# Performance work log

Measured on AMD Instinct MI355X. Metric: run time of the kernel, lower is better.

Reference implementation:

```python
import jax, jax.numpy as jnp
import numpy as np
from jax import lax

B, NPG, IN, OUT, ETYPES, STEPS, E = 16, 1024, 128, 256, 2, 6, 262144
N = B * NPG
CONCAT = IN + OUT
EPS = 1e-5


def setup_inputs() -> dict:
    key = jax.random.key(0)
    ks = jax.random.split(key, 24)
    s = 0.05
    return {
        "features": jax.random.normal(ks[0], (N, IN), jnp.float32),
        "src": jax.random.randint(ks[1], (E,), 0, N, jnp.int32),
        "dst": jax.random.randint(ks[2], (E,), 0, N, jnp.int32),
        "etype": jax.random.randint(ks[3], (E,), 0, ETYPES, jnp.int32),
        # GGNN per-etype linears (weight, bias) and GRUCell params
        "W_lin": jax.random.normal(ks[4], (ETYPES, OUT, OUT), jnp.float32) * s,
        "b_lin": jnp.zeros((ETYPES, OUT), jnp.float32),
        "W_ih": jax.random.normal(ks[5], (3 * OUT, OUT), jnp.float32) * s,
        "W_hh": jax.random.normal(ks[6], (3 * OUT, OUT), jnp.float32) * s,
        "b_ih": jnp.zeros((3 * OUT,), jnp.float32),
        "b_hh": jnp.zeros((3 * OUT,), jnp.float32),
        # conv branch on h_i (OUT channels)
        "conv1_w": jax.random.normal(ks[7], (OUT, OUT, 3), jnp.float32) * s,
        "conv1_b": jnp.zeros((OUT,), jnp.float32),
        "conv2_w": jax.random.normal(ks[8], (OUT, OUT, 1), jnp.float32) * s,
        "conv2_b": jnp.zeros((OUT,), jnp.float32),
        # conv branch on c_i (CONCAT channels)
        "convc1_w": jax.random.normal(ks[9], (CONCAT, CONCAT, 3), jnp.float32) * s,
        "convc1_b": jnp.zeros((CONCAT,), jnp.float32),
        "convc2_w": jax.random.normal(ks[10], (CONCAT, CONCAT, 1), jnp.float32) * s,
        "convc2_b": jnp.zeros((CONCAT,), jnp.float32),
        # shared batchnorms (training-mode batch stats, affine params)
        "bn_g": jnp.ones((OUT,), jnp.float32),
        "bn_b": jnp.zeros((OUT,), jnp.float32),
        "bnc_g": jnp.ones((CONCAT,), jnp.float32),
        "bnc_b": jnp.zeros((CONCAT,), jnp.float32),
        # gating MLPs
        "mlpy_w": jax.random.normal(ks[11], (2, OUT), jnp.float32) * s,
        "mlpy_b": jnp.zeros((2,), jnp.float32),
        "mlpz_w": jax.random.normal(ks[12], (2, CONCAT), jnp.float32) * s,
        "mlpz_b": jnp.zeros((2,), jnp.float32),
    }


def _bn_relu(x, g, b):  # x: [B, C, L], training-mode BN (biased var)
    mean = x.mean(axis=(0, 2), keepdims=True)
    var = ((x - mean) ** 2).mean(axis=(0, 2), keepdims=True)
    xn = (x - mean) * lax.rsqrt(var + EPS)
    return jax.nn.relu(xn * g[None, :, None] + b[None, :, None])


def _conv1d(x, w, b):  # x: [B, C, L], w: [O, I, K]
    y = lax.conv_general_dilated(x, w, (1,), 'VALID',
                                 dimension_numbers=('NCH', 'OIH', 'NCH'))
    return y + b[None, :, None]


def _maxpool(x, k, s):
    return lax.reduce_window(x, -jnp.inf, lax.max, (1, 1, k), (1, 1, s), 'VALID')


def _forward(features, src, dst, etype, W_lin, b_lin, W_ih, W_hh, b_ih, b_hh,
             conv1_w, conv1_b, conv2_w, conv2_b, convc1_w, convc1_b,
             convc2_w, convc2_b, bn_g, bn_b, bnc_g, bnc_b,
             mlpy_w, mlpy_b, mlpz_w, mlpz_b):
    # --- GatedGraphConv (DGL semantics): pad, n_steps of msg-pass + GRUCell ---
    h = jnp.pad(features, ((0, 0), (0, OUT - IN)))  # [N, OUT]
    for _ in range(STEPS):
        # per-etype linear applied to all nodes: [ETYPES, N, OUT]
        Wh = jnp.einsum('nd,ekd->enk', h, W_lin) + b_lin[:, None, :]
        msg = Wh[etype, src]                              # [E, OUT] gather
        agg = jax.ops.segment_sum(msg, dst, num_segments=N)  # scatter-add
        gi = agg @ W_ih.T + b_ih
        gh = h @ W_hh.T + b_hh
        ir, iz, ig = jnp.split(gi, 3, axis=-1)
        hr, hz, hg = jnp.split(gh, 3, axis=-1)
        r = jax.nn.sigmoid(ir + hr)
        z = jax.nn.sigmoid(iz + hz)
        n = jnp.tanh(ig + r * hg)
        h = (1.0 - z) * n + z * h

    h_i = h.reshape(B, NPG, OUT)
    x_i = features.reshape(B, NPG, IN)
    c_i = jnp.concatenate([h_i, x_i], axis=-1)  # [B, NPG, CONCAT]

    hT = jnp.swapaxes(h_i, 1, 2)  # [B, OUT, NPG]
    Y1 = _maxpool(_bn_relu(_conv1d(hT, conv1_w, conv1_b), bn_g, bn_b), 3, 2)
    Y2 = jnp.swapaxes(_maxpool(_bn_relu(_conv1d(Y1, conv2_w, conv2_b), bn_g, bn_b), 2, 2), 1, 2)

    cT = jnp.swapaxes(c_i, 1, 2)  # [B, CONCAT, NPG]
    Z1 = _maxpool(_bn_relu(_conv1d(cT, convc1_w, convc1_b), bnc_g, bnc_b), 3, 2)
    Z2 = jnp.swapaxes(_maxpool(_bn_relu(_conv1d(Z1, convc2_w, convc2_b), bnc_g, bnc_b), 2, 2), 1, 2)

    before_avg = (Y2 @ mlpy_w.T + mlpy_b) * (Z2 @ mlpz_w.T + mlpz_b)  # [B, L, 2]
    return jax.nn.sigmoid(before_avg.mean(axis=1))  # [B, 2]


def reference(features, src, dst, etype, W_lin, b_lin, W_ih, W_hh, b_ih, b_hh,
              conv1_w, conv1_b, conv2_w, conv2_b, convc1_w, convc1_b,
              convc2_w, convc2_b, bn_g, bn_b, bnc_g, bnc_b,
              mlpy_w, mlpy_b, mlpz_w, mlpz_b):
    return _forward(features, src, dst, etype, W_lin, b_lin, W_ih, W_hh, b_ih, b_hh,
                    conv1_w, conv1_b, conv2_w, conv2_b, convc1_w, convc1_b,
                    convc2_w, convc2_b, bn_g, bn_b, bnc_g, bnc_b,
                    mlpy_w, mlpy_b, mlpz_w, mlpz_b)
```

## Files before the change

### kernel.cpp

```cpp
#include <hip/hip_runtime.h>
#include <math.h>

constexpr int Bn     = 16;
constexpr int NPG    = 1024;
constexpr int Nn     = Bn * NPG;
constexpr int FIN    = 128;
constexpr int FOUT   = 256;
constexpr int CCAT   = 384;
constexpr int STEPS  = 6;
constexpr int NE     = 262144;

using short8 = __attribute__((ext_vector_type(8))) short;
using f32x4  = __attribute__((ext_vector_type(4))) float;

static __device__ __forceinline__ unsigned short f2bf(float x) {
    union { float f; unsigned u; } v; v.f = x;
    unsigned r = (v.u + 0x7FFFu + ((v.u >> 16) & 1u)) >> 16;
    return (unsigned short)r;
}
static __device__ __forceinline__ float bf2f(unsigned short b) {
    union { unsigned u; float f; } v; v.u = ((unsigned)b) << 16;
    return v.f;
}
static __device__ __forceinline__ float sigm(float x) { return 1.f / (1.f + expf(-x)); }

static __device__ __forceinline__ void gload16(const void* g, void* l) {
    __builtin_amdgcn_global_load_lds(
        (const __attribute__((address_space(1))) void*)g,
        (__attribute__((address_space(3))) void*)l, 16, 0, 0);
}


__global__ void cvt_bf(const float* __restrict__ s, unsigned short* __restrict__ d, int n) {
    int i = blockIdx.x * 256 + threadIdx.x;
    if (i < n) d[i] = f2bf(s[i]);
}

__global__ void cvt_wcat(const float* __restrict__ Wih, const float* __restrict__ Whh,
                         unsigned short* __restrict__ Wcat) {
    int o = blockIdx.x * 256 + threadIdx.x;
    int k = o >> 9, j = o & 511;
    float v = (j < 256) ? Whh[(size_t)k * 256 + j] : Wih[(size_t)k * 256 + (j - 256)];
    Wcat[o] = f2bf(v);
}

__global__ void add_bias(const float* __restrict__ a, const float* __restrict__ b,
                         float* __restrict__ o, int n) {
    int i = blockIdx.x * 256 + threadIdx.x;
    if (i < n) o[i] = a[i] + b[i];
}

__global__ void cvt_wconv(const float* __restrict__ W, unsigned short* __restrict__ Wt,
                          int C, int KW, int n) {
    int o = blockIdx.x * 256 + threadIdx.x;
    if (o >= n) return;
    int c = o / (KW * C), rem = o % (KW * C);
    int kb = rem / C, i = rem % C;
    Wt[o] = f2bf(W[(size_t)(c * C + i) * KW + kb]);
}

__global__ void pad_h(const float* __restrict__ f, float* __restrict__ h,
                      unsigned short* __restrict__ Acat) {
    int i = blockIdx.x * 256 + threadIdx.x;
    int k = i & 255, n = i >> 8;
    float v = (k < FIN) ? f[(size_t)n * FIN + k] : 0.f;
    h[i] = v; Acat[(size_t)n * 512 + k] = f2bf(v);
}

__global__ void build_cb(const unsigned short* __restrict__ Acat, const float* __restrict__ f,
                         unsigned short* __restrict__ cb) {
    int idx = blockIdx.x * 256 + threadIdx.x;
    int c = idx % CCAT, n = idx / CCAT;
    cb[idx] = (c < FOUT) ? Acat[(size_t)n * 512 + c] : f2bf(f[(size_t)n * FIN + (c - FOUT)]);
}


__global__ void edge_count(const int* __restrict__ dst, int* __restrict__ deg) {
    int e = blockIdx.x * 256 + threadIdx.x;
    atomicAdd(&deg[dst[e]], 1);
}

__global__ __launch_bounds__(1024) void scan_deg(const int* __restrict__ deg,
                                                 int* __restrict__ rowptr,
                                                 int* __restrict__ cursor) {
    __shared__ int ps[1024];
    const int t = threadIdx.x;
    int loc[16]; int s = 0;
    const int base = t * 16;
#pragma unroll
    for (int i = 0; i < 16; ++i) { loc[i] = deg[base + i]; s += loc[i]; }
    ps[t] = s;
    __syncthreads();
    for (int off = 1; off < 1024; off <<= 1) {
        int add = (t >= off) ? ps[t - off] : 0;
        __syncthreads();
        ps[t] += add;
        __syncthreads();
    }
    int run = ps[t] - s;
#pragma unroll
    for (int i = 0; i < 16; ++i) { rowptr[base + i] = run; cursor[base + i] = run; run += loc[i]; }
    if (t == 1023) rowptr[16384] = run;
}

__global__ void edge_fill(const int* __restrict__ src, const int* __restrict__ dst,
                          const int* __restrict__ et, int* __restrict__ cursor,
                          int* __restrict__ widx) {
    int e = blockIdx.x * 256 + threadIdx.x;
    int slot = atomicAdd(&cursor[dst[e]], 1);
    widx[slot] = src[e] * 2 + et[e];
}

static __device__ __forceinline__ void gemm128_body(
    const unsigned short* __restrict__ Ab, const unsigned short* __restrict__ W,
    const float* __restrict__ bias, float* __restrict__ Cf,
    unsigned short* __restrict__ Cb, int Ctap, int lda, int L, int Lv, int N, int K,
    int outBf, int l0, int col0, unsigned short* As, unsigned short* Bs) {
    const int t = threadIdx.x;
    const int w = t >> 6, l = t & 63;
    const int lr = l & 15, lhi = l >> 4;
    const int wr = w >> 1, wc = w & 1;
    const int srow8 = l >> 3;
    const int scole = ((l & 7) ^ srow8) * 8;
    const int lx7 = l & 7;

    f32x4 acc[4][4] = {};

    for (int k0 = 0; k0 < K; k0 += 64) {
        const int kb = k0 / Ctap;
        const int i0 = k0 - kb * Ctap;
        __syncthreads();
#pragma unroll
        for (int p = 0; p < 4; ++p) {
            const int r = w * 32 + p * 8;
            int srow = l0 + r + srow8 + kb;
            srow = srow < L ? srow : L - 1;
            gload16(Ab + (size_t)srow * lda + i0 + scole, &As[r * 64]);
            gload16(W + (size_t)(col0 + r + srow8) * K + k0 + scole, &Bs[r * 64]);
        }
        __syncthreads();
        const int abase = (wr * 64 + lr) * 64;
        const int bbase = (wc * 64 + lr) * 64;
#pragma unroll
        for (int kk = 0; kk < 2; ++kk) {
            const int soff = ((kk * 4 + lhi) ^ lx7) * 8;
            short8 af[4], bw[4];
#pragma unroll
            for (int fi = 0; fi < 4; ++fi)
                af[fi] = *(const short8*)&As[abase + fi * 1024 + soff];
#pragma unroll
            for (int fj = 0; fj < 4; ++fj)
                bw[fj] = *(const short8*)&Bs[bbase + fj * 1024 + soff];
#pragma unroll
            for (int fi = 0; fi < 4; ++fi)
#pragma unroll
                for (int fj = 0; fj < 4; ++fj)
                    acc[fi][fj] = __builtin_amdgcn_mfma_f32_16x16x32_bf16(
                        af[fi], bw[fj], acc[fi][fj], 0, 0, 0);
        }
    }
    const int rb = lhi * 4;
#pragma unroll
    for (int fi = 0; fi < 4; ++fi)
#pragma unroll
        for (int fj = 0; fj < 4; ++fj) {
            const int gcol = col0 + wc * 64 + fj * 16 + lr;
            const float bv = bias[gcol];
#pragma unroll
            for (int rr = 0; rr < 4; ++rr) {
                const int grow = l0 + wr * 64 + fi * 16 + rb + rr;
                if (grow < Lv) {
                    float v = acc[fi][fj][rr] + bv;
                    const size_t o = (size_t)grow * N + gcol;
                    if (outBf) Cb[o] = f2bf(v);
                    else       Cf[o] = v;
                }
            }
        }
}

__global__ __launch_bounds__(256) void gemm128(
    const unsigned short* __restrict__ A, const unsigned short* __restrict__ W,
    const float* __restrict__ bias, float* __restrict__ Cf,
    unsigned short* __restrict__ Cb, int Ctap, int lda, int L, int Lv, int N, int K,
    int outBf) {
    __shared__ unsigned short As[128 * 64];
    __shared__ unsigned short Bs[128 * 64];
    const size_t zo = (size_t)blockIdx.z;
    gemm128_body(A + zo * (size_t)L * lda, W, bias,
                 Cf ? Cf + zo * (size_t)Lv * N : nullptr,
                 Cb ? Cb + zo * (size_t)Lv * N : nullptr,
                 Ctap, lda, L, Lv, N, K, outBf,
                 blockIdx.y * 128, blockIdx.x * 128, As, Bs);
}

__global__ __launch_bounds__(256) void gemm128_swz(
    const unsigned short* __restrict__ A, const unsigned short* __restrict__ W,
    const float* __restrict__ bias, unsigned short* __restrict__ Cb,
    int lda, int N, int K) {
    __shared__ unsigned short As[128 * 64];
    __shared__ unsigned short Bs[128 * 64];
    const int gX = gridDim.x;
    const int hId = blockIdx.x + gX * blockIdx.y;
    const int xcd = hId & 7, tt = hId >> 3;
    const int bx = tt % gX, by = xcd + 8 * (tt / gX);
    gemm128_body(A, W, bias, nullptr, Cb, lda, lda, Nn, Nn, N, K, 1,
                 by * 128, bx * 128, As, Bs);
}

__global__ __launch_bounds__(256) void gemm_gru(
    const unsigned short* __restrict__ Acat, const unsigned short* __restrict__ Wcat,
    const unsigned short* __restrict__ Whg, const float* __restrict__ bias_s,
    const float* __restrict__ bias_g, float* __restrict__ h,
    unsigned short* __restrict__ Anext) {
    __shared__ unsigned short As[64 * 64];
    __shared__ unsigned short Bs[256 * 64];
    const int hId = blockIdx.x + 4 * blockIdx.y;
    const int xcd = hId & 7, tt = hId >> 3;
    const int bx = tt & 3, by = xcd + 8 * (tt >> 2);
    const int l0 = by * 64, c0 = bx * 64;

    const int t = threadIdx.x;
    const int w = t >> 6, l = t & 63;
    const int lr = l & 15, lhi = l >> 4;
    const int srow8 = l >> 3;
    const int scole = ((l & 7) ^ srow8) * 8;
    const int lx7 = l & 7;

    f32x4 acc[16] = {};

#pragma unroll
    for (int k0 = 0; k0 < 512; k0 += 64) {
        __syncthreads();
#pragma unroll
        for (int p = 0; p < 2; ++p) {
            const int r = w * 16 + p * 8;
            gload16(Acat + (size_t)(l0 + r + srow8) * 512 + k0 + scole, &As[r * 64]);
        }
#pragma unroll
        for (int p = 0; p < 8; ++p) {
            const int r = w * 64 + p * 8;
            if (r < 192) {
                const int g = r >> 6;
                const int cr = (r & 63) + srow8;
                gload16(Wcat + (size_t)(g * 256 + c0 + cr) * 512 + k0 + scole, &Bs[r * 64]);
            } else if (k0 < 256) {
                const int cr = (r - 192) + srow8;
                gload16(Whg + (size_t)(c0 + cr) * 256 + k0 + scole, &Bs[r * 64]);
            }
        }
        __syncthreads();
        const int abase = (w * 16 + lr) * 64;
#pragma unroll
        for (int kk = 0; kk < 2; ++kk) {
            const int soff = ((kk * 4 + lhi) ^ lx7) * 8;
            short8 a0 = *(const short8*)&As[abase + soff];
#pragma unroll
            for (int g = 0; g < 4; ++g) {
                if (!(g == 3 && k0 >= 256)) {
#pragma unroll
                    for (int fj = 0; fj < 4; ++fj) {
                        short8 bb = *(const short8*)&Bs[(g * 64 + fj * 16 + lr) * 64 + soff];
                        acc[g * 4 + fj] = __builtin_amdgcn_mfma_f32_16x16x32_bf16(
                            a0, bb, acc[g * 4 + fj], 0, 0, 0);
                    }
                }
            }
        }
    }
    const int rb = lhi * 4;
#pragma unroll
    for (int fj = 0; fj < 4; ++fj) {
        const int c = c0 + fj * 16 + lr;
        const float br = bias_s[c];
        const float bz = bias_s[256 + c];
        const float bg = bias_s[512 + c];
        const float bh = bias_g[c];
#pragma unroll
        for (int rr = 0; rr < 4; ++rr) {
            const int grow = l0 + w * 16 + rb + rr;
            float sr = acc[0 * 4 + fj][rr] + br;
            float sz = acc[1 * 4 + fj][rr] + bz;
            float sg = acc[2 * 4 + fj][rr] + bg;
            float hg = acc[3 * 4 + fj][rr] + bh;
            float r = sigm(sr), z = sigm(sz);
            float nn = tanhf(sg - (1.f - r) * hg);
            const size_t ho = (size_t)grow * 256 + c;
            float hv = (1.f - z) * nn + z * h[ho];
            h[ho] = hv;
            Anext[(size_t)grow * 512 + c] = f2bf(hv);
        }
    }
}

__global__ __launch_bounds__(64) void gather_agg(
    const unsigned short* __restrict__ Whb, const int* __restrict__ rowptr,
    const int* __restrict__ widx, unsigned short* __restrict__ Acat) {
    const int n = blockIdx.x, t = threadIdx.x;
    float a0 = 0, a1 = 0, a2 = 0, a3 = 0;
    const int s0 = rowptr[n], s1 = rowptr[n + 1];
    for (int s = s0; s < s1; ++s) {
        const ushort4 v = *(const ushort4*)(Whb + (size_t)widx[s] * 256 + t * 4);
        a0 += bf2f(v.x); a1 += bf2f(v.y); a2 += bf2f(v.z); a3 += bf2f(v.w);
    }
    ushort4 o; o.x = f2bf(a0); o.y = f2bf(a1); o.z = f2bf(a2); o.w = f2bf(a3);
    *(ushort4*)(Acat + (size_t)n * 512 + 256 + t * 4) = o;
}

constexpr int NCHUNK = 128;
__global__ __launch_bounds__(256) void bn_part_cl(
    const float* __restrict__ X, float* __restrict__ pS, float* __restrict__ pQ,
    int C, int totalRows, int rowsPerChunk) {
    const int t  = threadIdx.x;
    const int cq = t & 31, rl = t >> 5;
    const int c0 = blockIdx.x * 128 + cq * 4;
    const int r0 = blockIdx.y * rowsPerChunk;
    const int r1 = min(r0 + rowsPerChunk, totalRows);
    float s0 = 0, s1 = 0, s2 = 0, s3 = 0, q0 = 0, q1 = 0, q2 = 0, q3 = 0;
    for (int r = r0 + rl; r < r1; r += 8) {
        float4 v = *(const float4*)(X + (size_t)r * C + c0);
        s0 += v.x; s1 += v.y; s2 += v.z; s3 += v.w;
        q0 += v.x * v.x; q1 += v.y * v.y; q2 += v.z * v.z; q3 += v.w * v.w;
    }
    __shared__ float ls[8][128], lq[8][128];
    ls[rl][cq * 4 + 0] = s0; ls[rl][cq * 4 + 1] = s1;
    ls[rl][cq * 4 + 2] = s2; ls[rl][cq * 4 + 3] = s3;
    lq[rl][cq * 4 + 0] = q0; lq[rl][cq * 4 + 1] = q1;
    lq[rl][cq * 4 + 2] = q2; lq[rl][cq * 4 + 3] = q3;
    __syncthreads();
    if (rl == 0) {
#pragma unroll
        for (int i = 0; i < 4; ++i) {
            const int c = cq * 4 + i;
            float ss = 0, qq = 0;
#pragma unroll
            for (int j = 0; j < 8; ++j) { ss += ls[j][c]; qq += lq[j][c]; }
            pS[(size_t)blockIdx.y * C + c0 + i] = ss;
            pQ[(size_t)blockIdx.y * C + c0 + i] = qq;
        }
    }
}

__global__ __launch_bounds__(128) void bn_reduce_cl(
    const float* __restrict__ pS, const float* __restrict__ pQ,
    float* __restrict__ mean, float* __restrict__ var, int C, int totalRows) {
    const int c = blockIdx.x, t = threadIdx.x;
    __shared__ float rs[128], rq[128];
    rs[t] = pS[(size_t)t * C + c];
    rq[t] = pQ[(size_t)t * C + c];
    __syncthreads();
    for (int st = 64; st; st >>= 1) {
        if (t < st) { rs[t] += rs[t + st]; rq[t] += rq[t + st]; }
        __syncthreads();
    }
    if (t == 0) {
        float m = rs[0] / totalRows;
        mean[c] = m;
        var[c]  = rq[0] / totalRows - m * m;
    }
}

__global__ void bnp_cl(const float* __restrict__ X, const float* __restrict__ mean,
                       const float* __restrict__ var, const float* __restrict__ g,
                       const float* __restrict__ bta, float* __restrict__ Of,
                       unsigned short* __restrict__ Ob, int C, int Lin, int Lout,
                       int Kp, int outBf) {
    int idx = blockIdx.x * 256 + threadIdx.x;
    if (idx >= Bn * Lout * C) return;
    int c = idx % C, j = (idx / C) % Lout, b = idx / (C * Lout);
    float sc = g[c] * rsqrtf(var[c] + 1e-5f);
    float sh = bta[c] - mean[c] * sc;
    const float* xb = X + ((size_t)b * Lin + j * 2) * C + c;
    float m = 0.f;
    for (int k = 0; k < Kp; ++k) m = fmaxf(m, xb[(size_t)k * C] * sc + sh);
    if (outBf) Ob[idx] = f2bf(m);
    else       Of[idx] = m;
}

__global__ void final_dot(const float* __restrict__ Y2, const float* __restrict__ Z2,
                          const float* __restrict__ wy, const float* __restrict__ by,
                          const float* __restrict__ wz, const float* __restrict__ bz,
                          float* __restrict__ prod) {
    const int b = blockIdx.y, j = blockIdx.x, t = threadIdx.x;
    float p0 = 0, p1 = 0, q0 = 0, q1 = 0;
    const float* yrow = Y2 + (size_t)(b * 255 + j) * FOUT;
    const float* zrow = Z2 + (size_t)(b * 255 + j) * CCAT;
    for (int c = t; c < FOUT; c += 128) {
        float v = yrow[c];
        p0 += v * wy[c]; p1 += v * wy[FOUT + c];
    }
    for (int c = t; c < CCAT; c += 128) {
        float v = zrow[c];
        q0 += v * wz[c]; q1 += v * wz[CCAT + c];
    }
    __shared__ float r0[128], r1[128], r2[128], r3[128];
    r0[t] = p0; r1[t] = p1; r2[t] = q0; r3[t] = q1;
    __syncthreads();
    for (int s = 64; s; s >>= 1) {
        if (t < s) { r0[t] += r0[t + s]; r1[t] += r1[t + s]; r2[t] += r2[t + s]; r3[t] += r3[t + s]; }
        __syncthreads();
    }
    if (t == 0) {
        float y0 = r0[0] + by[0], y1 = r1[0] + by[1];
        float z0 = r2[0] + bz[0], z1 = r3[0] + bz[1];
        prod[((size_t)b * 255 + j) * 2 + 0] = y0 * z0;
        prod[((size_t)b * 255 + j) * 2 + 1] = y1 * z1;
    }
}

__global__ void final_out(const float* __restrict__ prod, float* __restrict__ out) {
    const int b = blockIdx.x, t = threadIdx.x;
    const int w = t >> 6, lane = t & 63;
    float s = 0.f;
    for (int j = lane; j < 255; j += 64) s += prod[((size_t)b * 255 + j) * 2 + w];
#pragma unroll
    for (int off = 32; off; off >>= 1) s += __shfl_down(s, off);
    if (lane == 0) out[b * 2 + w] = 1.f / (1.f + expf(-s / 255.f));
}

extern "C" void kernel_launch(void* const* d_in, const int* in_sizes, int n_in,
                              void* d_out, int out_size, void* d_ws, size_t ws_size,
                              hipStream_t stream) {
    (void)in_sizes; (void)n_in; (void)out_size; (void)ws_size;
    const float* features = (const float*)d_in[0];
    const int*   src      = (const int*)d_in[1];
    const int*   dst      = (const int*)d_in[2];
    const int*   etype    = (const int*)d_in[3];
    const float* W_lin    = (const float*)d_in[4];
    const float* b_lin    = (const float*)d_in[5];
    const float* W_ih     = (const float*)d_in[6];
    const float* W_hh     = (const float*)d_in[7];
    const float* b_ih     = (const float*)d_in[8];
    const float* b_hh     = (const float*)d_in[9];
    const float* conv1_w  = (const float*)d_in[10];
    const float* conv1_b  = (const float*)d_in[11];
    const float* conv2_w  = (const float*)d_in[12];
    const float* conv2_b  = (const float*)d_in[13];
    const float* convc1_w = (const float*)d_in[14];
    const float* convc1_b = (const float*)d_in[15];
    const float* convc2_w = (const float*)d_in[16];
    const float* convc2_b = (const float*)d_in[17];
    const float* bn_g     = (const float*)d_in[18];
    const float* bn_b     = (const float*)d_in[19];
    const float* bnc_g    = (const float*)d_in[20];
    const float* bnc_b    = (const float*)d_in[21];
    const float* mlpy_w   = (const float*)d_in[22];
    const float* mlpy_b   = (const float*)d_in[23];
    const float* mlpz_w   = (const float*)d_in[24];
    const float* mlpz_b   = (const float*)d_in[25];

    float* ws = (float*)d_ws;
    float*          h      = ws;
    unsigned short* Acat0  = (unsigned short*)(ws + 4194304);
    float*          bufA   = ws + 8388608;
    float*          bufB   = ws + 20971520;
    unsigned short* Wlin_b = (unsigned short*)(ws + 33554432);
    unsigned short* Whh_b  = (unsigned short*)(ws + 33554432) + 131072;
    unsigned short* Wcat_b = (unsigned short*)(ws + 33554432) + 327680;
    float*          bias_s = ws + 33950000;
    int*            ib     = (int*)(ws + 34000000);
    int* deg    = ib;
    int* cursor = ib + 16384;
    int* rowptr = ib + 32768;
    int* widx   = ib + 49160;
    float* sreg = ws + 34500000;
    float* meanb = sreg;
    float* varb  = sreg + 384;
    float* pS    = sreg + 1024;
    float* pQ    = sreg + 50176;
    float* prod  = sreg + 99328;

    unsigned short* Whb   = (unsigned short*)bufA;
    unsigned short* Acat1 = (unsigned short*)(bufA + 4194304);
    const unsigned short* Whg = Whh_b + 512 * 256;

    cvt_bf<<<512,  256, 0, stream>>>(W_lin, Wlin_b, 131072);
    cvt_bf<<<768,  256, 0, stream>>>(W_hh,  Whh_b,  196608);
    cvt_wcat<<<1536, 256, 0, stream>>>(W_ih, W_hh, Wcat_b);
    add_bias<<<3, 256, 0, stream>>>(b_ih, b_hh, bias_s, 768);
    pad_h<<<Nn * FOUT / 256, 256, 0, stream>>>(features, h, Acat0);

    hipMemsetAsync(deg, 0, 16384 * sizeof(int), stream);
    edge_count<<<NE / 256, 256, 0, stream>>>(dst, deg);
    scan_deg<<<1, 1024, 0, stream>>>(deg, rowptr, cursor);
    edge_fill<<<NE / 256, 256, 0, stream>>>(src, dst, etype, cursor, widx);

    unsigned short* Acur = Acat0;
    unsigned short* Anxt = Acat1;
    for (int s6 = 0; s6 < STEPS; ++s6) {
        gemm128_swz<<<dim3(4, 128), 256, 0, stream>>>(
            Acur, Wlin_b, b_lin, Whb, 512, 512, 256);
        gather_agg<<<Nn, 64, 0, stream>>>(Whb, rowptr, widx, Acur);
        gemm_gru<<<dim3(4, 256), 256, 0, stream>>>(
            Acur, Wcat_b, Whg, bias_s, b_hh + 512, h, Anxt);
        unsigned short* tmp = Acur; Acur = Anxt; Anxt = tmp;
    }

    unsigned short* cb    = (unsigned short*)ws;
    float*          Yc1   = bufA;
    unsigned short* P1y   = (unsigned short*)(bufA + 4186112);
    float*          Yc2   = bufA + 5230592;
    float*          Y2    = bufA + 7319552;
    float*          Z2    = bufA + 8364032;
    float*          Zc1   = bufB;
    unsigned short* P1z   = (unsigned short*)(bufB + 6279168);
    float*          Zc2   = bufB + 7845888;
    unsigned short* Wcv   = (unsigned short*)(bufB + 11000000);
    unsigned short* c1b   = Wcv;
    unsigned short* c2b   = Wcv + 196608;
    unsigned short* cc1b  = Wcv + 262144;
    unsigned short* cc2b  = Wcv + 704512;

    cvt_wconv<<<768,  256, 0, stream>>>(conv1_w,  c1b,  FOUT, 3, FOUT * FOUT * 3);
    cvt_wconv<<<256,  256, 0, stream>>>(conv2_w,  c2b,  FOUT, 1, FOUT * FOUT);
    cvt_wconv<<<1728, 256, 0, stream>>>(convc1_w, cc1b, CCAT, 3, CCAT * CCAT * 3);
    cvt_wconv<<<576,  256, 0, stream>>>(convc2_w, cc2b, CCAT, 1, CCAT * CCAT);
    build_cb<<<Nn * CCAT / 256, 256, 0, stream>>>(Acat0, features, cb);

    const int rows1 = Bn * 1022;
    const int rows2 = Bn * 510;
    const int rpc1  = (rows1 + NCHUNK - 1) / NCHUNK;
    const int rpc2  = (rows2 + NCHUNK - 1) / NCHUNK;

    gemm128<<<dim3(2, 8, Bn), 256, 0, stream>>>(Acat0, c1b, conv1_b, Yc1, nullptr,
                                                FOUT, 512, 1024, 1022, FOUT, 768, 0);
    bn_part_cl<<<dim3(FOUT / 128, NCHUNK), 256, 0, stream>>>(Yc1, pS, pQ, FOUT, rows1, rpc1);
    bn_reduce_cl<<<FOUT, 128, 0, stream>>>(pS, pQ, meanb, varb, FOUT, rows1);
    bnp_cl<<<(Bn * 510 * FOUT + 255) / 256, 256, 0, stream>>>(
        Yc1, meanb, varb, bn_g, bn_b, nullptr, P1y, FOUT, 1022, 510, 3, 1);
    gemm128<<<dim3(2, 4, Bn), 256, 0, stream>>>(P1y, c2b, conv2_b, Yc2, nullptr,
                                                FOUT, 256, 510, 510, FOUT, 256, 0);
    bn_part_cl<<<dim3(FOUT / 128, NCHUNK), 256, 0, stream>>>(Yc2, pS, pQ, FOUT, rows2, rpc2);
    bn_reduce_cl<<<FOUT, 128, 0, stream>>>(pS, pQ, meanb, varb, FOUT, rows2);
    bnp_cl<<<(Bn * 255 * FOUT + 255) / 256, 256, 0, stream>>>(
        Yc2, meanb, varb, bn_g, bn_b, Y2, nullptr, FOUT, 510, 255, 2, 0);

    gemm128<<<dim3(3, 8, Bn), 256, 0, stream>>>(cb, cc1b, convc1_b, Zc1, nullptr,
                                                CCAT, 384, 1024, 1022, CCAT, 1152, 0);
    bn_part_cl<<<dim3(CCAT / 128, NCHUNK), 256, 0, stream>>>(Zc1, pS, pQ, CCAT, rows1, rpc1);
    bn_reduce_cl<<<CCAT, 128, 0, stream>>>(pS, pQ, meanb, varb, CCAT, rows1);
    bnp_cl<<<(Bn * 510 * CCAT + 255) / 256, 256, 0, stream>>>(
        Zc1, meanb, varb, bnc_g, bnc_b, nullptr, P1z, CCAT, 1022, 510, 3, 1);
    gemm128<<<dim3(3, 4, Bn), 256, 0, stream>>>(P1z, cc2b, convc2_b, Zc2, nullptr,
                                                CCAT, 384, 510, 510, CCAT, 384, 0);
    bn_part_cl<<<dim3(CCAT / 128, NCHUNK), 256, 0, stream>>>(Zc2, pS, pQ, CCAT, rows2, rpc2);
    bn_reduce_cl<<<CCAT, 128, 0, stream>>>(pS, pQ, meanb, varb, CCAT, rows2);
    bnp_cl<<<(Bn * 255 * CCAT + 255) / 256, 256, 0, stream>>>(
        Zc2, meanb, varb, bnc_g, bnc_b, Z2, nullptr, CCAT, 510, 255, 2, 0);

    final_dot<<<dim3(255, Bn), 128, 0, stream>>>(Y2, Z2, mlpy_w, mlpy_b, mlpz_w, mlpz_b, prod);
    final_out<<<Bn, 128, 0, stream>>>(prod, (float*)d_out);
}
```

Baseline: 683.8 us.

## Fold per-etype linear into GRU input weights and aggregate raw hidden states

Uses linearity to precompute W_ih·W_lin[t] per edge type and a degree-weighted bias term, so each step only gathers and sums raw h per edge type and then runs one GRU GEMM with K=768. This drops the per-step 16384x512x256 message GEMM and its write-back of the transformed messages. In exchange the GRU GEMM K grows from 512 to 768, the gather writes two sums, and rounding to bf16 now happens at a different point, which shifts numerical error.

```diff
diff --git a/kernel.cpp b/kernel.cpp
--- a/kernel.cpp
+++ b/kernel.cpp
@@ -36,12 +36,32 @@
     if (i < n) d[i] = f2bf(s[i]);
 }
 
-__global__ void cvt_wcat(const float* __restrict__ Wih, const float* __restrict__ Whh,
-                         unsigned short* __restrict__ Wcat) {
-    int o = blockIdx.x * 256 + threadIdx.x;
-    int k = o >> 9, j = o & 511;
-    float v = (j < 256) ? Whh[(size_t)k * 256 + j] : Wih[(size_t)k * 256 + (j - 256)];
-    Wcat[o] = f2bf(v);
+__global__ void build_wbig(const float* __restrict__ Wih, const float* __restrict__ Whh,
+                           const float* __restrict__ Wlin, unsigned short* __restrict__ Wbig) {
+    int idx = blockIdx.x * 256 + threadIdx.x;
+    int n = idx / 768, k = idx % 768;
+    float v;
+    if (k < 256) {
+        v = Whh[(size_t)n * 256 + k];
+    } else {
+        int t = (k < 512) ? 0 : 1;
+        int d = k - 256 - t * 256;
+        const float* wl = Wlin + (size_t)t * 65536;
+        float s = 0.f;
+        for (int j = 0; j < 256; ++j) s += Wih[(size_t)n * 256 + j] * wl[(size_t)j * 256 + d];
+        v = s;
+    }
+    Wbig[idx] = f2bf(v);
+}
+
+__global__ void build_bv(const float* __restrict__ Wih, const float* __restrict__ blin,
+                         float* __restrict__ bv) {
+    int i = blockIdx.x * 256 + threadIdx.x;
+    if (i >= 1536) return;
+    int t = i / 768, n = i % 768;
+    float s = 0.f;
+    for (int k = 0; k < 256; ++k) s += Wih[(size_t)n * 256 + k] * blin[t * 256 + k];
+    bv[i] = s;
 }
 
 __global__ void add_bias(const float* __restrict__ a, const float* __restrict__ b,
@@ -64,20 +84,22 @@
     int i = blockIdx.x * 256 + threadIdx.x;
     int k = i & 255, n = i >> 8;
     float v = (k < FIN) ? f[(size_t)n * FIN + k] : 0.f;
-    h[i] = v; Acat[(size_t)n * 512 + k] = f2bf(v);
+    h[i] = v; Acat[(size_t)n * 768 + k] = f2bf(v);
 }
 
 __global__ void build_cb(const unsigned short* __restrict__ Acat, const float* __restrict__ f,
                          unsigned short* __restrict__ cb) {
     int idx = blockIdx.x * 256 + threadIdx.x;
     int c = idx % CCAT, n = idx / CCAT;
-    cb[idx] = (c < FOUT) ? Acat[(size_t)n * 512 + c] : f2bf(f[(size_t)n * FIN + (c - FOUT)]);
-}
-
-
-__global__ void edge_count(const int* __restrict__ dst, int* __restrict__ deg) {
+    cb[idx] = (c < FOUT) ? Acat[(size_t)n * 768 + c] : f2bf(f[(size_t)n * FIN + (c - FOUT)]);
+}
+
+
+__global__ void edge_count(const int* __restrict__ dst, const int* __restrict__ et,
+                           int* __restrict__ deg, int* __restrict__ degt) {
     int e = blockIdx.x * 256 + threadIdx.x;
     atomicAdd(&deg[dst[e]], 1);
+    atomicAdd(&degt[dst[e] * 2 + et[e]], 1);
 }
 
 __global__ __launch_bounds__(1024) void scan_deg(const int* __restrict__ deg,
@@ -109,6 +131,13 @@
     int e = blockIdx.x * 256 + threadIdx.x;
     int slot = atomicAdd(&cursor[dst[e]], 1);
     widx[slot] = src[e] * 2 + et[e];
+}
+
+__global__ void degt_to_f(const int* __restrict__ degt, float* __restrict__ d0,
+                          float* __restrict__ d1) {
+    int n = blockIdx.x * 256 + threadIdx.x;
+    d0[n] = (float)degt[2 * n];
+    d1[n] = (float)degt[2 * n + 1];
 }
 
 static __device__ __forceinline__ void gemm128_body(
@@ -194,25 +223,35 @@
                  blockIdx.y * 128, blockIdx.x * 128, As, Bs);
 }
 
-__global__ __launch_bounds__(256) void gemm128_swz(
-    const unsigned short* __restrict__ A, const unsigned short* __restrict__ W,
-    const float* __restrict__ bias, unsigned short* __restrict__ Cb,
-    int lda, int N, int K) {
-    __shared__ unsigned short As[128 * 64];
-    __shared__ unsigned short Bs[128 * 64];
-    const int gX = gridDim.x;
-    const int hId = blockIdx.x + gX * blockIdx.y;
-    const int xcd = hId & 7, tt = hId >> 3;
-    const int bx = tt % gX, by = xcd + 8 * (tt / gX);
-    gemm128_body(A, W, bias, nullptr, Cb, lda, lda, Nn, Nn, N, K, 1,
-                 by * 128, bx * 128, As, Bs);
+__global__ __launch_bounds__(64) void gather_S(
+    const int* __restrict__ rowptr, const int* __restrict__ widx,
+    unsigned short* __restrict__ Acat) {
+    const int n = blockIdx.x, t = threadIdx.x;
+    float a0 = 0, a1 = 0, a2 = 0, a3 = 0;
+    float b0 = 0, b1 = 0, b2 = 0, b3 = 0;
+    const int s0 = rowptr[n], s1 = rowptr[n + 1];
+    for (int s = s0; s < s1; ++s) {
+        const int wi = widx[s];
+        const ushort4 v = *(const ushort4*)(Acat + (size_t)(wi >> 1) * 768 + t * 4);
+        if ((wi & 1) == 0) {
+            a0 += bf2f(v.x); a1 += bf2f(v.y); a2 += bf2f(v.z); a3 += bf2f(v.w);
+        } else {
+            b0 += bf2f(v.x); b1 += bf2f(v.y); b2 += bf2f(v.z); b3 += bf2f(v.w);
+        }
+    }
+    ushort4 oa, ob;
+    oa.x = f2bf(a0); oa.y = f2bf(a1); oa.z = f2bf(a2); oa.w = f2bf(a3);
+    ob.x = f2bf(b0); ob.y = f2bf(b1); ob.z = f2bf(b2); ob.w = f2bf(b3);
+    *(ushort4*)(Acat + (size_t)n * 768 + 256 + t * 4) = oa;
+    *(ushort4*)(Acat + (size_t)n * 768 + 512 + t * 4) = ob;
 }
 
 __global__ __launch_bounds__(256) void gemm_gru(
-    const unsigned short* __restrict__ Acat, const unsigned short* __restrict__ Wcat,
+    const unsigned short* __restrict__ Acat, const unsigned short* __restrict__ Wbig,
     const unsigned short* __restrict__ Whg, const float* __restrict__ bias_s,
-    const float* __restrict__ bias_g, float* __restrict__ h,
-    unsigned short* __restrict__ Anext) {
+    const float* __restrict__ bias_g, const float* __restrict__ bv,
+    const float* __restrict__ deg0f, const float* __restrict__ deg1f,
+    float* __restrict__ h, unsigned short* __restrict__ Anext) {
     __shared__ unsigned short As[64 * 64];
     __shared__ unsigned short Bs[256 * 64];
     const int hId = blockIdx.x + 4 * blockIdx.y;
@@ -230,12 +269,12 @@
     f32x4 acc[16] = {};
 
 #pragma unroll
-    for (int k0 = 0; k0 < 512; k0 += 64) {
+    for (int k0 = 0; k0 < 768; k0 += 64) {
         __syncthreads();
 #pragma unroll
         for (int p = 0; p < 2; ++p) {
             const int r = w * 16 + p * 8;
-            gload16(Acat + (size_t)(l0 + r + srow8) * 512 + k0 + scole, &As[r * 64]);
+            gload16(Acat + (size_t)(l0 + r + srow8) * 768 + k0 + scole, &As[r * 64]);
         }
 #pragma unroll
         for (int p = 0; p < 8; ++p) {
@@ -243,7 +282,7 @@
             if (r < 192) {
                 const int g = r >> 6;
                 const int cr = (r & 63) + srow8;
-                gload16(Wcat + (size_t)(g * 256 + c0 + cr) * 512 + k0 + scole, &Bs[r * 64]);
+                gload16(Wbig + (size_t)(g * 256 + c0 + cr) * 768 + k0 + scole, &Bs[r * 64]);
             } else if (k0 < 256) {
                 const int cr = (r - 192) + srow8;
                 gload16(Whg + (size_t)(c0 + cr) * 256 + k0 + scole, &Bs[r * 64]);
@@ -270,41 +309,24 @@
     }
     const int rb = lhi * 4;
 #pragma unroll
-    for (int fj = 0; fj < 4; ++fj) {
-        const int c = c0 + fj * 16 + lr;
-        const float br = bias_s[c];
-        const float bz = bias_s[256 + c];
-        const float bg = bias_s[512 + c];
-        const float bh = bias_g[c];
-#pragma unroll
-        for (int rr = 0; rr < 4; ++rr) {
-            const int grow = l0 + w * 16 + rb + rr;
-            float sr = acc[0 * 4 + fj][rr] + br;
-            float sz = acc[1 * 4 + fj][rr] + bz;
-            float sg = acc[2 * 4 + fj][rr] + bg;
-            float hg = acc[3 * 4 + fj][rr] + bh;
+    for (int rr = 0; rr < 4; ++rr) {
+        const int grow = l0 + w * 16 + rb + rr;
+        const float d0 = deg0f[grow], d1 = deg1f[grow];
+#pragma unroll
+        for (int fj = 0; fj < 4; ++fj) {
+            const int c = c0 + fj * 16 + lr;
+            float sr = acc[0 * 4 + fj][rr] + bias_s[c]       + d0 * bv[c]       + d1 * bv[768 + c];
+            float sz = acc[1 * 4 + fj][rr] + bias_s[256 + c] + d0 * bv[256 + c] + d1 * bv[1024 + c];
+            float sg = acc[2 * 4 + fj][rr] + bias_s[512 + c] + d0 * bv[512 + c] + d1 * bv[1280 + c];
+            float hg = acc[3 * 4 + fj][rr] + bias_g[c];
             float r = sigm(sr), z = sigm(sz);
             float nn = tanhf(sg - (1.f - r) * hg);
             const size_t ho = (size_t)grow * 256 + c;
             float hv = (1.f - z) * nn + z * h[ho];
             h[ho] = hv;
-            Anext[(size_t)grow * 512 + c] = f2bf(hv);
-        }
-    }
-}
-
-__global__ __launch_bounds__(64) void gather_agg(
-    const unsigned short* __restrict__ Whb, const int* __restrict__ rowptr,
-    const int* __restrict__ widx, unsigned short* __restrict__ Acat) {
-    const int n = blockIdx.x, t = threadIdx.x;
-    float a0 = 0, a1 = 0, a2 = 0, a3 = 0;
-    const int s0 = rowptr[n], s1 = rowptr[n + 1];
-    for (int s = s0; s < s1; ++s) {
-        const ushort4 v = *(const ushort4*)(Whb + (size_t)widx[s] * 256 + t * 4);
-        a0 += bf2f(v.x); a1 += bf2f(v.y); a2 += bf2f(v.z); a3 += bf2f(v.w);
-    }
-    ushort4 o; o.x = f2bf(a0); o.y = f2bf(a1); o.z = f2bf(a2); o.w = f2bf(a3);
-    *(ushort4*)(Acat + (size_t)n * 512 + 256 + t * 4) = o;
+            Anext[(size_t)grow * 768 + c] = f2bf(hv);
+        }
+    }
 }
 
 constexpr int NCHUNK = 128;
@@ -452,47 +474,46 @@
     float* ws = (float*)d_ws;
     float*          h      = ws;
     unsigned short* Acat0  = (unsigned short*)(ws + 4194304);
-    float*          bufA   = ws + 8388608;
-    float*          bufB   = ws + 20971520;
-    unsigned short* Wlin_b = (unsigned short*)(ws + 33554432);
-    unsigned short* Whh_b  = (unsigned short*)(ws + 33554432) + 131072;
-    unsigned short* Wcat_b = (unsigned short*)(ws + 33554432) + 327680;
-    float*          bias_s = ws + 33950000;
-    int*            ib     = (int*)(ws + 34000000);
-    int* deg    = ib;
-    int* cursor = ib + 16384;
-    int* rowptr = ib + 32768;
-    int* widx   = ib + 49160;
-    float* sreg = ws + 34500000;
-    float* meanb = sreg;
-    float* varb  = sreg + 384;
-    float* pS    = sreg + 1024;
-    float* pQ    = sreg + 50176;
-    float* prod  = sreg + 99328;
-
-    unsigned short* Whb   = (unsigned short*)bufA;
-    unsigned short* Acat1 = (unsigned short*)(bufA + 4194304);
-    const unsigned short* Whg = Whh_b + 512 * 256;
-
-    cvt_bf<<<512,  256, 0, stream>>>(W_lin, Wlin_b, 131072);
-    cvt_bf<<<768,  256, 0, stream>>>(W_hh,  Whh_b,  196608);
-    cvt_wcat<<<1536, 256, 0, stream>>>(W_ih, W_hh, Wcat_b);
+    float*          bufA   = ws + 10485760;
+    unsigned short* Acat1  = (unsigned short*)bufA;
+    float*          bufB   = ws + 23068672;
+
+    int* deg    = (int*)(ws + 17485760);
+    int* degt   = deg + 16384;
+    int* cursor = degt + 32768;
+    int* rowptr = cursor + 16384;
+    int* widx   = rowptr + 16400;
+    float* deg0f = ws + 17830000;
+    float* deg1f = ws + 17846384;
+    unsigned short* Wbig_b = (unsigned short*)(ws + 17900000);
+    unsigned short* Whg_b  = (unsigned short*)(ws + 18200000);
+    float* bias_s = ws + 18240000;
+    float* bv     = ws + 18240768;
+
+    float* meanb = ws + 20485760;
+    float* varb  = meanb + 384;
+    float* pS    = ws + 20486784;
+    float* pQ    = ws + 20535936;
+    float* prod  = ws + 20585088;
+
+    cvt_bf<<<256, 256, 0, stream>>>(W_hh + 512 * 256, Whg_b, 65536);
+    build_wbig<<<2304, 256, 0, stream>>>(W_ih, W_hh, W_lin, Wbig_b);
+    build_bv<<<6, 256, 0, stream>>>(W_ih, b_lin, bv);
     add_bias<<<3, 256, 0, stream>>>(b_ih, b_hh, bias_s, 768);
     pad_h<<<Nn * FOUT / 256, 256, 0, stream>>>(features, h, Acat0);
 
-    hipMemsetAsync(deg, 0, 16384 * sizeof(int), stream);
-    edge_count<<<NE / 256, 256, 0, stream>>>(dst, deg);
+    hipMemsetAsync(deg, 0, 49152 * sizeof(int), stream);
+    edge_count<<<NE / 256, 256, 0, stream>>>(dst, etype, deg, degt);
     scan_deg<<<1, 1024, 0, stream>>>(deg, rowptr, cursor);
     edge_fill<<<NE / 256, 256, 0, stream>>>(src, dst, etype, cursor, widx);
+    degt_to_f<<<64, 256, 0, stream>>>(degt, deg0f, deg1f);
 
     unsigned short* Acur = Acat0;
     unsigned short* Anxt = Acat1;
     for (int s6 = 0; s6 < STEPS; ++s6) {
-        gemm128_swz<<<dim3(4, 128), 256, 0, stream>>>(
-            Acur, Wlin_b, b_lin, Whb, 512, 512, 256);
-        gather_agg<<<Nn, 64, 0, stream>>>(Whb, rowptr, widx, Acur);
+        gather_S<<<Nn, 64, 0, stream>>>(rowptr, widx, Acur);
         gemm_gru<<<dim3(4, 256), 256, 0, stream>>>(
-            Acur, Wcat_b, Whg, bias_s, b_hh + 512, h, Anxt);
+            Acur, Wbig_b, Whg_b, bias_s, b_hh + 512, bv, deg0f, deg1f, h, Anxt);
         unsigned short* tmp = Acur; Acur = Anxt; Anxt = tmp;
     }
 
@@ -523,7 +544,7 @@
     const int rpc2  = (rows2 + NCHUNK - 1) / NCHUNK;
 
     gemm128<<<dim3(2, 8, Bn), 256, 0, stream>>>(Acat0, c1b, conv1_b, Yc1, nullptr,
-                                                FOUT, 512, 1024, 1022, FOUT, 768, 0);
+                                                FOUT, 768, 1024, 1022, FOUT, 768, 0);
     bn_part_cl<<<dim3(FOUT / 128, NCHUNK), 256, 0, stream>>>(Yc1, pS, pQ, FOUT, rows1, rpc1);
     bn_reduce_cl<<<FOUT, 128, 0, stream>>>(pS, pQ, meanb, varb, FOUT, rows1);
     bnp_cl<<<(Bn * 510 * FOUT + 255) / 256, 256, 0, stream>>>(
```

Result: slower. 739.6 us (+8.2%).
